# Kernel optimization log

Hardware: AMD Instinct MI355X
Metric: run time of the kernel (lower is better)

## Reference

```python
import jax, jax.numpy as jnp
import numpy as np

B = 256          # graphs per batch
N = 128          # nodes per graph (equal-size graphs; batch is block-contiguous)
P = N * (N - 1) // 2  # pairs per graph = 8128
E = B * 1024     # total edges
D = 128          # node feature dim
L = 32           # latent dim

# precomputed local upper-triangular pair indices (constants)
_PI, _PJ = np.triu_indices(N, k=1)
_PI = jnp.asarray(_PI); _PJ = jnp.asarray(_PJ)


def setup_inputs() -> dict:
    key = jax.random.key(0)
    ks = jax.random.split(key, 8)
    x = jax.random.normal(ks[0], (B * N, D), dtype=jnp.float32)
    # within-graph edges with local i < j
    li = jax.random.randint(ks[1], (E,), 0, N - 1)
    r = jax.random.randint(ks[2], (E,), 0, 1 << 30)
    lj = li + 1 + r % (N - 1 - li)
    g = jax.random.randint(ks[3], (E,), 0, B)
    off = g * N
    edge_index = jnp.stack([off + li, off + lj]).astype(jnp.int64)
    batch = jnp.repeat(jnp.arange(B), N).astype(jnp.int64)
    eps = jax.random.normal(ks[4], (B * N, L), dtype=jnp.float32)
    W1 = jax.random.normal(ks[5], (D, D), dtype=jnp.float32) * 0.05
    b1 = jnp.zeros((D,), dtype=jnp.float32)
    Wmu = jax.random.normal(ks[6], (D, L), dtype=jnp.float32) * 0.05
    bmu = jnp.zeros((L,), dtype=jnp.float32)
    Wls = jax.random.normal(ks[7], (D, L), dtype=jnp.float32) * 0.05
    bls = jnp.zeros((L,), dtype=jnp.float32)
    return {"x": x, "edge_index": edge_index, "batch": batch, "eps": eps,
            "W1": W1, "b1": b1, "Wmu": Wmu, "bmu": bmu, "Wls": Wls, "bls": bls}


def reference(x, edge_index, batch, eps, W1, b1, Wmu, bmu, Wls, bls):
    src, dst = edge_index[0], edge_index[1]
    # --- encoder: one symmetric message-passing layer -> Gaussian q per node ---
    agg = jnp.zeros_like(x).at[dst].add(x[src]).at[src].add(x[dst])
    h = jax.nn.relu((x + agg) @ W1 + b1)
    mu = h @ Wmu + bmu                       # [BN, L]
    log_std = h @ Wls + bls
    std = jnp.exp(log_std)
    z = mu + std * eps                       # rsample
    # --- KL(q || N(0,I)) per node, summed per graph (kls[b]) ---
    kl_node = 0.5 * jnp.sum(std * std + mu * mu - 1.0 - 2.0 * log_std, axis=-1)
    kls = jax.ops.segment_sum(kl_node, batch, num_segments=B)  # [B]
    # --- link targets: scatter edges into triangular pair slots ---
    li, lj, be = src % N, dst % N, src // N
    pidx = li * (2 * N - li - 1) // 2 + (lj - li - 1)
    targets = jnp.zeros((B, P), dtype=z.dtype).at[be, pidx].set(1.0)
    # --- inner-product Bernoulli decoder over all pairs of every graph ---
    zb = z.reshape(B, N, L)
    logits = jnp.einsum('bpl,bpl->bp', zb[:, _PI], zb[:, _PJ])   # [B, P]
    log_probs = jnp.sum(targets * logits - jax.nn.softplus(logits), axis=-1)  # [B]
    elbo = jnp.mean(log_probs - kls)
    return -elbo
```

## Files before the change

kernel.cpp:

```cpp
#include <hip/hip_runtime.h>
#include <math.h>

#define B_ 256
#define N_ 128
#define D_ 128
#define L_ 32
#define E_ 262144
#define PW_ 254
#define DCAP 96

#define NDEG_OFF 0
#define BM_OFF   32768
#define KLS_OFF  97792
#define LP_OFF   98048
#define ADJ_OFF  98304
#define Z_OFF    884736
#define ZERO_WORDS 98304

__global__ __launch_bounds__(256) void k_build(
    const int* __restrict__ ei, unsigned* __restrict__ ndeg,
    unsigned char* __restrict__ adj, unsigned* __restrict__ bm)
{
    int e0 = (blockIdx.x * 256 + threadIdx.x) * 2;
    int2 s2 = *(const int2*)(ei + e0);
    int2 d2 = *(const int2*)(ei + E_ + e0);
    #pragma unroll
    for (int u = 0; u < 2; ++u) {
        int src = u ? s2.y : s2.x;
        int dst = u ? d2.y : d2.x;
        unsigned s1 = atomicAdd(&ndeg[src], 1u);
        if (s1 < DCAP) adj[(size_t)src * DCAP + s1] = (unsigned char)(dst & 127);
        unsigned s2a = atomicAdd(&ndeg[dst], 1u);
        if (s2a < DCAP) adj[(size_t)dst * DCAP + s2a] = (unsigned char)(src & 127);
        int li = src & 127, lj = dst & 127, g = src >> 7;
        int p = li * (255 - li) / 2 + (lj - li - 1);
        atomicOr(&bm[g * PW_ + (p >> 5)], 1u << (p & 31));
    }
}

__global__ __launch_bounds__(256, 4) void k_encoder(
    const float* __restrict__ x, const unsigned* __restrict__ ndeg,
    const unsigned char* __restrict__ adj,
    const float* __restrict__ W1, const float* __restrict__ b1,
    const float* __restrict__ Wmu, const float* __restrict__ bmu,
    const float* __restrict__ Wls, const float* __restrict__ bls,
    const float* __restrict__ eps,
    float* __restrict__ z, float* __restrict__ kls)
{
    __shared__ float XAs[32 * 132];
    __shared__ float Ws[4096];
    int t = threadIdx.x;
    int g = blockIdx.x & 255;
    int quar = blockIdx.x >> 8;
    int row0 = g * 128 + quar * 32;
    int rg = t >> 5;
    int cg = t & 31;
    int lane = t & 63;

    {
        int nidx = t >> 4;
        int fo = (t & 15) * 8;
        for (int p = 0; p < 2; ++p) {
            int lrow = p * 16 + nidx;
            int gnode = row0 + lrow;
            const float* xr = x + (size_t)gnode * 128 + fo;
            float4 a0 = *(const float4*)xr;
            float4 a1 = *(const float4*)(xr + 4);
            int deg = (int)ndeg[gnode];
            if (deg > DCAP) deg = DCAP;
            const unsigned char* al = adj + (size_t)gnode * DCAP;
            const float* gx = x + (size_t)(gnode & ~127) * 128 + fo;
            int e = 0;
            for (; e + 4 <= deg; e += 4) {
                unsigned pk = *(const unsigned*)(al + e);
                const float* r0 = gx + (pk & 255u) * 128;
                const float* r1 = gx + ((pk >> 8) & 255u) * 128;
                const float* r2 = gx + ((pk >> 16) & 255u) * 128;
                const float* r3 = gx + (pk >> 24) * 128;
                float4 v00 = *(const float4*)r0, v01 = *(const float4*)(r0 + 4);
                float4 v10 = *(const float4*)r1, v11 = *(const float4*)(r1 + 4);
                float4 v20 = *(const float4*)r2, v21 = *(const float4*)(r2 + 4);
                float4 v30 = *(const float4*)r3, v31 = *(const float4*)(r3 + 4);
                a0.x += v00.x + v10.x + v20.x + v30.x;
                a0.y += v00.y + v10.y + v20.y + v30.y;
                a0.z += v00.z + v10.z + v20.z + v30.z;
                a0.w += v00.w + v10.w + v20.w + v30.w;
                a1.x += v01.x + v11.x + v21.x + v31.x;
                a1.y += v01.y + v11.y + v21.y + v31.y;
                a1.z += v01.z + v11.z + v21.z + v31.z;
                a1.w += v01.w + v11.w + v21.w + v31.w;
            }
            for (; e < deg; ++e) {
                const float* r = gx + (unsigned)al[e] * 128;
                float4 v0 = *(const float4*)r, v1 = *(const float4*)(r + 4);
                a0.x += v0.x; a0.y += v0.y; a0.z += v0.z; a0.w += v0.w;
                a1.x += v1.x; a1.y += v1.y; a1.z += v1.z; a1.w += v1.w;
            }
            *(float4*)(XAs + lrow * 132 + fo) = a0;
            *(float4*)(XAs + lrow * 132 + fo + 4) = a1;
        }
    }
    __syncthreads();

    float acc[4][4];
    #pragma unroll
    for (int i = 0; i < 4; ++i)
        #pragma unroll
        for (int j = 0; j < 4; ++j) acc[i][j] = 0.f;

    for (int kq = 0; kq < 4; ++kq) {
        if (kq) __syncthreads();
        #pragma unroll
        for (int i = 0; i < 4; ++i) {
            int c = t + i * 256;
            ((float4*)Ws)[c] = ((const float4*)(W1 + kq * 4096))[c];
        }
        __syncthreads();
        #pragma unroll 2
        for (int k = 0; k < 32; k += 4) {
            float4 av[4], wv[4];
            #pragma unroll
            for (int i = 0; i < 4; ++i)
                av[i] = *(const float4*)(XAs + (4 * rg + i) * 132 + kq * 32 + k);
            #pragma unroll
            for (int dk = 0; dk < 4; ++dk)
                wv[dk] = *(const float4*)(Ws + (k + dk) * 128 + 4 * cg);
            #pragma unroll
            for (int i = 0; i < 4; ++i) {
                acc[i][0] += av[i].x * wv[0].x + av[i].y * wv[1].x + av[i].z * wv[2].x + av[i].w * wv[3].x;
                acc[i][1] += av[i].x * wv[0].y + av[i].y * wv[1].y + av[i].z * wv[2].y + av[i].w * wv[3].y;
                acc[i][2] += av[i].x * wv[0].z + av[i].y * wv[1].z + av[i].z * wv[2].z + av[i].w * wv[3].z;
                acc[i][3] += av[i].x * wv[0].w + av[i].y * wv[1].w + av[i].z * wv[2].w + av[i].w * wv[3].w;
            }
        }
    }
    __syncthreads();

    {
        float4 bb = *(const float4*)(b1 + 4 * cg);
        #pragma unroll
        for (int i = 0; i < 4; ++i) {
            float4 h;
            h.x = fmaxf(acc[i][0] + bb.x, 0.f);
            h.y = fmaxf(acc[i][1] + bb.y, 0.f);
            h.z = fmaxf(acc[i][2] + bb.z, 0.f);
            h.w = fmaxf(acc[i][3] + bb.w, 0.f);
            *(float4*)(XAs + (4 * rg + i) * 132 + 4 * cg) = h;
        }
    }

    float a3[4][2];
    #pragma unroll
    for (int i = 0; i < 4; ++i) { a3[i][0] = 0.f; a3[i][1] = 0.f; }

    for (int kh = 0; kh < 2; ++kh) {
        __syncthreads();
        #pragma unroll
        for (int i = 0; i < 4; ++i) {
            int c = t + i * 256;
            int row = c >> 4, col4 = (c & 15) << 2;
            int rowg = kh * 64 + row;
            float4 v = (col4 < 32) ? *(const float4*)(Wmu + rowg * 32 + col4)
                                   : *(const float4*)(Wls + rowg * 32 + col4 - 32);
            *(float4*)(Ws + row * 64 + col4) = v;
        }
        __syncthreads();
        #pragma unroll 2
        for (int k = 0; k < 64; k += 4) {
            float4 av[4];
            float2 wv[4];
            #pragma unroll
            for (int i = 0; i < 4; ++i)
                av[i] = *(const float4*)(XAs + (4 * rg + i) * 132 + kh * 64 + k);
            #pragma unroll
            for (int dk = 0; dk < 4; ++dk)
                wv[dk] = *(const float2*)(Ws + (k + dk) * 64 + 2 * cg);
            #pragma unroll
            for (int i = 0; i < 4; ++i) {
                a3[i][0] += av[i].x * wv[0].x + av[i].y * wv[1].x + av[i].z * wv[2].x + av[i].w * wv[3].x;
                a3[i][1] += av[i].x * wv[0].y + av[i].y * wv[1].y + av[i].z * wv[2].y + av[i].w * wv[3].y;
            }
        }
    }
    {
        float2 bv = (cg < 16) ? *(const float2*)(bmu + 2 * cg)
                              : *(const float2*)(bls + 2 * cg - 32);
        #pragma unroll
        for (int i = 0; i < 4; ++i) { a3[i][0] += bv.x; a3[i][1] += bv.y; }
    }

    float o3[4][2];
    #pragma unroll
    for (int i = 0; i < 4; ++i) {
        o3[i][0] = __shfl_xor(a3[i][0], 16);
        o3[i][1] = __shfl_xor(a3[i][1], 16);
    }

    float klsum = 0.f;
    if (cg < 16) {
        int lo = cg;
        #pragma unroll
        for (int i = 0; i < 4; ++i) {
            int rowg = row0 + 4 * rg + i;
            float mu0 = a3[i][0], mu1 = a3[i][1];
            float ls0 = o3[i][0], ls1 = o3[i][1];
            float2 ev = *(const float2*)(eps + (size_t)rowg * 32 + 2 * lo);
            float s0 = __expf(ls0), s1 = __expf(ls1);
            float2 zv = make_float2(mu0 + s0 * ev.x, mu1 + s1 * ev.y);
            *(float2*)(z + (size_t)rowg * 32 + 2 * lo) = zv;
            klsum += s0 * s0 + mu0 * mu0 - 1.f - 2.f * ls0
                   + s1 * s1 + mu1 * mu1 - 1.f - 2.f * ls1;
        }
    }
    #pragma unroll
    for (int off = 32; off > 0; off >>= 1) klsum += __shfl_xor(klsum, off);
    if (lane == 0) atomicAdd(&kls[g], 0.5f * klsum);
}

__global__ __launch_bounds__(256) void k_decoder(
    const float* __restrict__ z, const unsigned* __restrict__ bitmap,
    float* __restrict__ logp)
{
    __shared__ float zT[32 * 132];
    __shared__ unsigned bm[PW_];
    int b = blockIdx.x & 255, quar = blockIdx.x >> 8, t = threadIdx.x;

    #pragma unroll
    for (int i = 0; i < 4; ++i) {
        int c = t + i * 256;
        int n = c >> 3, l = (c & 7) << 2;
        float4 v = *(const float4*)(z + ((size_t)b * N_ + n) * L_ + l);
        zT[(l + 0) * 132 + n] = v.x;
        zT[(l + 1) * 132 + n] = v.y;
        zT[(l + 2) * 132 + n] = v.z;
        zT[(l + 3) * 132 + n] = v.w;
    }
    if (t < PW_) bm[t] = bitmap[b * PW_ + t];
    __syncthreads();

    int i0 = quar * 32 + ((t >> 5) << 2);
    int j0 = (t & 31) << 2;
    float g[4][4];
    #pragma unroll
    for (int a = 0; a < 4; ++a)
        #pragma unroll
        for (int c = 0; c < 4; ++c) g[a][c] = 0.f;

    #pragma unroll 4
    for (int l = 0; l < 32; ++l) {
        float4 a0 = *(const float4*)(zT + l * 132 + i0);
        float4 b0 = *(const float4*)(zT + l * 132 + j0);
        float za[4] = {a0.x, a0.y, a0.z, a0.w};
        float zb[4] = {b0.x, b0.y, b0.z, b0.w};
        #pragma unroll
        for (int a = 0; a < 4; ++a)
            #pragma unroll
            for (int c = 0; c < 4; ++c) g[a][c] += za[a] * zb[c];
    }

    float sum = 0.f;
    #pragma unroll
    for (int a = 0; a < 4; ++a) {
        int i = i0 + a;
        #pragma unroll
        for (int c = 0; c < 4; ++c) {
            int j = j0 + c;
            if (j > i) {
                float lg = g[a][c];
                int p = i * (255 - i) / 2 + (j - i - 1);
                unsigned bit = (bm[p >> 5] >> (p & 31)) & 1u;
                float sp = __logf(1.f + __expf(-fabsf(lg))) + fmaxf(lg, 0.f);
                sum += bit ? (lg - sp) : (-sp);
            }
        }
    }
    #pragma unroll
    for (int off = 32; off > 0; off >>= 1) sum += __shfl_xor(sum, off);
    if ((t & 63) == 0) atomicAdd(&logp[b], sum);
}

__global__ __launch_bounds__(256) void k_finalize(
    const float* __restrict__ kls, const float* __restrict__ logp,
    float* __restrict__ out)
{
    __shared__ float RED[256];
    int t = threadIdx.x;
    RED[t] = logp[t] - kls[t];
    __syncthreads();
    for (int s = 128; s > 0; s >>= 1) {
        if (t < s) RED[t] += RED[t + s];
        __syncthreads();
    }
    if (t == 0) out[0] = -RED[0] * (1.0f / 256.0f);
}

extern "C" void kernel_launch(void* const* d_in, const int* in_sizes, int n_in,
                              void* d_out, int out_size, void* d_ws, size_t ws_size,
                              hipStream_t stream) {
    const float* x   = (const float*)d_in[0];
    const int*   ei  = (const int*)d_in[1];
    const float* eps = (const float*)d_in[3];
    const float* W1  = (const float*)d_in[4];
    const float* b1  = (const float*)d_in[5];
    const float* Wmu = (const float*)d_in[6];
    const float* bmu = (const float*)d_in[7];
    const float* Wls = (const float*)d_in[8];
    const float* bls = (const float*)d_in[9];

    unsigned* wsw = (unsigned*)d_ws;
    unsigned*      ndeg = wsw + NDEG_OFF;
    unsigned*      bm   = wsw + BM_OFF;
    float*         kls  = (float*)(wsw + KLS_OFF);
    float*         logp = (float*)(wsw + LP_OFF);
    unsigned char* adj  = (unsigned char*)(wsw + ADJ_OFF);
    float*         z    = (float*)(wsw + Z_OFF);

    hipMemsetAsync(d_ws, 0, ZERO_WORDS * sizeof(unsigned), stream);

    k_build   <<<E_ / 512, 256, 0, stream>>>(ei, ndeg, adj, bm);
    k_encoder <<<1024, 256, 0, stream>>>(x, ndeg, adj, W1, b1, Wmu, bmu,
                                         Wls, bls, eps, z, kls);
    k_decoder <<<4 * B_, 256, 0, stream>>>(z, bm, logp);
    k_finalize<<<1, 256, 0, stream>>>(kls, logp, (float*)d_out);
}
```

Before: 179.8 us.

## Double-buffer encoder weight tiles in LDS and widen edge loads in build

The encoder's W1 and Wmu/Wls staging changes from load-sync-compute phases to a two-buffer pipeline. The next weight chunk is fetched into registers while the current chunk is being multiplied, then written to the other LDS buffer, so each chunk needs one barrier instead of two. The last W1 iteration prefetches the first Wmu/Wls chunk. Separately, k_build reads four edges per thread with int4 loads and launches half as many blocks. This adds register pressure and uses more, smaller chunks.

Measured after the change: 280.3 us. 55.9% more time.

```diff
diff --git a/kernel.cpp b/kernel.cpp
--- a/kernel.cpp
+++ b/kernel.cpp
@@ -21,17 +21,18 @@
     const int* __restrict__ ei, unsigned* __restrict__ ndeg,
     unsigned char* __restrict__ adj, unsigned* __restrict__ bm)
 {
-    int e0 = (blockIdx.x * 256 + threadIdx.x) * 2;
-    int2 s2 = *(const int2*)(ei + e0);
-    int2 d2 = *(const int2*)(ei + E_ + e0);
-    #pragma unroll
-    for (int u = 0; u < 2; ++u) {
-        int src = u ? s2.y : s2.x;
-        int dst = u ? d2.y : d2.x;
-        unsigned s1 = atomicAdd(&ndeg[src], 1u);
-        if (s1 < DCAP) adj[(size_t)src * DCAP + s1] = (unsigned char)(dst & 127);
-        unsigned s2a = atomicAdd(&ndeg[dst], 1u);
-        if (s2a < DCAP) adj[(size_t)dst * DCAP + s2a] = (unsigned char)(src & 127);
+    int e0 = (blockIdx.x * 256 + threadIdx.x) * 4;
+    int4 s4 = *(const int4*)(ei + e0);
+    int4 d4 = *(const int4*)(ei + E_ + e0);
+    int ss[4] = {s4.x, s4.y, s4.z, s4.w};
+    int dd[4] = {d4.x, d4.y, d4.z, d4.w};
+    #pragma unroll
+    for (int u = 0; u < 4; ++u) {
+        int src = ss[u], dst = dd[u];
+        unsigned a1 = atomicAdd(&ndeg[src], 1u);
+        if (a1 < DCAP) adj[(size_t)src * DCAP + a1] = (unsigned char)(dst & 127);
+        unsigned a2 = atomicAdd(&ndeg[dst], 1u);
+        if (a2 < DCAP) adj[(size_t)dst * DCAP + a2] = (unsigned char)(src & 127);
         int li = src & 127, lj = dst & 127, g = src >> 7;
         int p = li * (255 - li) / 2 + (lj - li - 1);
         atomicOr(&bm[g * PW_ + (p >> 5)], 1u << (p & 31));
@@ -100,6 +101,12 @@
             *(float4*)(XAs + lrow * 132 + fo + 4) = a1;
         }
     }
+    {
+        const float4* gp = (const float4*)W1;
+        float4 s0 = gp[t], s1 = gp[t + 256];
+        ((float4*)Ws)[t] = s0;
+        ((float4*)Ws)[t + 256] = s1;
+    }
     __syncthreads();
 
     float acc[4][4];
@@ -108,23 +115,31 @@
         #pragma unroll
         for (int j = 0; j < 4; ++j) acc[i][j] = 0.f;
 
-    for (int kq = 0; kq < 4; ++kq) {
-        if (kq) __syncthreads();
-        #pragma unroll
-        for (int i = 0; i < 4; ++i) {
-            int c = t + i * 256;
-            ((float4*)Ws)[c] = ((const float4*)(W1 + kq * 4096))[c];
-        }
-        __syncthreads();
-        #pragma unroll 2
-        for (int k = 0; k < 32; k += 4) {
+    #pragma unroll 1
+    for (int c = 0; c < 8; ++c) {
+        const float* wrd = Ws + ((c & 1) << 11);
+        float* wwr = Ws + (((c + 1) & 1) << 11);
+        float4 s0, s1;
+        if (c < 7) {
+            const float4* gp = (const float4*)(W1 + (c + 1) * 2048);
+            s0 = gp[t]; s1 = gp[t + 256];
+        } else {
+            int c0_ = (t & 15) << 2, c1_ = ((t + 256) & 15) << 2;
+            int r0_ = t >> 4, r1_ = (t + 256) >> 4;
+            s0 = (c0_ < 32) ? *(const float4*)(Wmu + r0_ * 32 + c0_)
+                            : *(const float4*)(Wls + r0_ * 32 + c0_ - 32);
+            s1 = (c1_ < 32) ? *(const float4*)(Wmu + r1_ * 32 + c1_)
+                            : *(const float4*)(Wls + r1_ * 32 + c1_ - 32);
+        }
+        #pragma unroll
+        for (int kk = 0; kk < 16; kk += 4) {
             float4 av[4], wv[4];
             #pragma unroll
             for (int i = 0; i < 4; ++i)
-                av[i] = *(const float4*)(XAs + (4 * rg + i) * 132 + kq * 32 + k);
+                av[i] = *(const float4*)(XAs + (4 * rg + i) * 132 + c * 16 + kk);
             #pragma unroll
             for (int dk = 0; dk < 4; ++dk)
-                wv[dk] = *(const float4*)(Ws + (k + dk) * 128 + 4 * cg);
+                wv[dk] = *(const float4*)(wrd + (kk + dk) * 128 + 4 * cg);
             #pragma unroll
             for (int i = 0; i < 4; ++i) {
                 acc[i][0] += av[i].x * wv[0].x + av[i].y * wv[1].x + av[i].z * wv[2].x + av[i].w * wv[3].x;
@@ -133,8 +148,10 @@
                 acc[i][3] += av[i].x * wv[0].w + av[i].y * wv[1].w + av[i].z * wv[2].w + av[i].w * wv[3].w;
             }
         }
-    }
-    __syncthreads();
+        ((float4*)wwr)[t] = s0;
+        ((float4*)wwr)[t + 256] = s1;
+        __syncthreads();
+    }
 
     {
         float4 bb = *(const float4*)(b1 + 4 * cg);
@@ -148,38 +165,46 @@
             *(float4*)(XAs + (4 * rg + i) * 132 + 4 * cg) = h;
         }
     }
+    __syncthreads();
 
     float a3[4][2];
     #pragma unroll
     for (int i = 0; i < 4; ++i) { a3[i][0] = 0.f; a3[i][1] = 0.f; }
 
-    for (int kh = 0; kh < 2; ++kh) {
-        __syncthreads();
-        #pragma unroll
-        for (int i = 0; i < 4; ++i) {
-            int c = t + i * 256;
-            int row = c >> 4, col4 = (c & 15) << 2;
-            int rowg = kh * 64 + row;
-            float4 v = (col4 < 32) ? *(const float4*)(Wmu + rowg * 32 + col4)
-                                   : *(const float4*)(Wls + rowg * 32 + col4 - 32);
-            *(float4*)(Ws + row * 64 + col4) = v;
-        }
-        __syncthreads();
-        #pragma unroll 2
-        for (int k = 0; k < 64; k += 4) {
+    #pragma unroll 1
+    for (int c2 = 0; c2 < 4; ++c2) {
+        const float* wrd = Ws + ((c2 & 1) << 11);
+        float* wwr = Ws + (((c2 + 1) & 1) << 11);
+        float4 s0, s1;
+        if (c2 < 3) {
+            int c0_ = (t & 15) << 2, c1_ = ((t + 256) & 15) << 2;
+            int r0_ = (c2 + 1) * 32 + (t >> 4);
+            int r1_ = (c2 + 1) * 32 + ((t + 256) >> 4);
+            s0 = (c0_ < 32) ? *(const float4*)(Wmu + r0_ * 32 + c0_)
+                            : *(const float4*)(Wls + r0_ * 32 + c0_ - 32);
+            s1 = (c1_ < 32) ? *(const float4*)(Wmu + r1_ * 32 + c1_)
+                            : *(const float4*)(Wls + r1_ * 32 + c1_ - 32);
+        }
+        #pragma unroll
+        for (int kk = 0; kk < 32; kk += 4) {
             float4 av[4];
             float2 wv[4];
             #pragma unroll
             for (int i = 0; i < 4; ++i)
-                av[i] = *(const float4*)(XAs + (4 * rg + i) * 132 + kh * 64 + k);
+                av[i] = *(const float4*)(XAs + (4 * rg + i) * 132 + c2 * 32 + kk);
             #pragma unroll
             for (int dk = 0; dk < 4; ++dk)
-                wv[dk] = *(const float2*)(Ws + (k + dk) * 64 + 2 * cg);
+                wv[dk] = *(const float2*)(wrd + (kk + dk) * 64 + 2 * cg);
             #pragma unroll
             for (int i = 0; i < 4; ++i) {
                 a3[i][0] += av[i].x * wv[0].x + av[i].y * wv[1].x + av[i].z * wv[2].x + av[i].w * wv[3].x;
                 a3[i][1] += av[i].x * wv[0].y + av[i].y * wv[1].y + av[i].z * wv[2].y + av[i].w * wv[3].y;
             }
+        }
+        if (c2 < 3) {
+            ((float4*)wwr)[t] = s0;
+            ((float4*)wwr)[t + 256] = s1;
+            __syncthreads();
         }
     }
     {
@@ -317,7 +342,7 @@
 
     hipMemsetAsync(d_ws, 0, ZERO_WORDS * sizeof(unsigned), stream);
 
-    k_build   <<<E_ / 512, 256, 0, stream>>>(ei, ndeg, adj, bm);
+    k_build   <<<E_ / 1024, 256, 0, stream>>>(ei, ndeg, adj, bm);
     k_encoder <<<1024, 256, 0, stream>>>(x, ndeg, adj, W1, b1, Wmu, bmu,
                                          Wls, bls, eps, z, kls);
     k_decoder <<<4 * B_, 256, 0, stream>>>(z, bm, logp);
```
